# Optimization experiments

Hardware: AMD Instinct MI355X
Metric: run time of the kernel (lower is better)

The kernel has to match this reference:

```python
import jax, jax.numpy as jnp
import numpy as np

D_MODEL = 1024
D_STATE = 16
D_CONV = 4
EXPAND = 2
D_INNER = EXPAND * D_MODEL          # 2048
DT_RANK = D_MODEL // 16             # 64 (math.ceil(d_model/16))
BATCH, SEQLEN = 2, 1024


def setup_inputs() -> dict:
    key = jax.random.key(0)
    ks = jax.random.split(key, 9)
    f32 = jnp.float32
    hidden_states = jax.random.normal(ks[0], (BATCH, SEQLEN, D_MODEL), dtype=f32)
    in_proj_w = jax.random.normal(ks[1], (2 * D_INNER, D_MODEL), dtype=f32) * (D_MODEL ** -0.5)
    conv1d_w = jax.random.normal(ks[2], (D_INNER, D_CONV), dtype=f32) * (D_CONV ** -0.5)
    conv1d_b = jax.random.normal(ks[3], (D_INNER,), dtype=f32) * 0.1
    x_proj_w = jax.random.normal(ks[4], (DT_RANK + 2 * D_STATE, D_INNER), dtype=f32) * (D_INNER ** -0.5)
    dt_std = DT_RANK ** -0.5
    dt_proj_w = jax.random.uniform(ks[5], (D_INNER, DT_RANK), dtype=f32, minval=-dt_std, maxval=dt_std)
    dt_proj_b = jax.random.normal(ks[6], (D_INNER,), dtype=f32) * 0.1
    # A = repeat(arange(1, d_state+1), 'n -> d n'); A_log = log(A)
    A_log = jnp.log(jnp.tile(jnp.arange(1, D_STATE + 1, dtype=f32), (D_INNER, 1)))
    D_param = jnp.ones((D_INNER,), dtype=f32)
    out_proj_w = jax.random.normal(ks[7], (D_MODEL, D_INNER), dtype=f32) * (D_INNER ** -0.5)
    return dict(hidden_states=hidden_states, in_proj_w=in_proj_w, conv1d_w=conv1d_w,
                conv1d_b=conv1d_b, x_proj_w=x_proj_w, dt_proj_w=dt_proj_w,
                dt_proj_b=dt_proj_b, A_log=A_log, D_param=D_param, out_proj_w=out_proj_w)


def _mamba_fwd(hidden_states, in_proj_w, conv1d_w, conv1d_b, x_proj_w,
               dt_proj_w, dt_proj_b, A_log, D_param, out_proj_w):
    Bsz, L, _ = hidden_states.shape
    # in_proj: (B,L,d_model) -> (B,L,2*d_inner); split into x, z
    xz = jnp.einsum('bld,ed->ble', hidden_states, in_proj_w)
    x, z = jnp.split(xz, 2, axis=-1)                      # each (B,L,d_inner)
    # causal depthwise conv1d over L (left pad d_conv-1), then SiLU (fused in causal_conv1d_fwd)
    xc = jnp.transpose(x, (0, 2, 1))                      # (B,d_inner,L)
    kern = conv1d_w[:, None, :]                           # (d_inner,1,d_conv)
    conv = jax.lax.conv_general_dilated(
        xc, kern, window_strides=(1,), padding=[(D_CONV - 1, 0)],
        dimension_numbers=('NCH', 'OIH', 'NCH'), feature_group_count=D_INNER)
    u = jax.nn.silu(conv + conv1d_b[None, :, None])       # (B,d_inner,L)
    ut = jnp.transpose(u, (0, 2, 1))                      # (B,L,d_inner)
    # x_proj -> [dt | B | C]
    x_dbl = jnp.einsum('bld,rd->blr', ut, x_proj_w)       # (B,L,dt_rank+2*d_state)
    dt_low = x_dbl[..., :DT_RANK]
    B_var = x_dbl[..., DT_RANK:DT_RANK + D_STATE]         # (B,L,d_state)
    C_var = x_dbl[..., DT_RANK + D_STATE:]                # (B,L,d_state)
    # delta = softplus(dt_proj_w @ dt_low + dt_proj_b)  (delta_bias applied inside selective scan)
    delta = jax.nn.softplus(jnp.einsum('blr,dr->bld', dt_low, dt_proj_w) + dt_proj_b)  # (B,L,d_inner)
    A = -jnp.exp(A_log)                                   # (d_inner,d_state)
    # discretize: h_l = exp(delta*A) * h_{l-1} + (delta*B_l) * u_l
    dA = jnp.exp(delta[..., None] * A)                    # (B,L,d_inner,d_state)
    dBu = delta[..., None] * B_var[:, :, None, :] * ut[..., None]  # (B,L,d_inner,d_state)

    def step(h, inp):
        da, dbu, c = inp
        h = da * h + dbu                                  # (B,d_inner,d_state)
        y = jnp.einsum('bdn,bn->bd', h, c)
        return h, y

    h0 = jnp.zeros((Bsz, D_INNER, D_STATE), dtype=hidden_states.dtype)
    _, ys = jax.lax.scan(step, h0, (jnp.moveaxis(dA, 1, 0),
                                    jnp.moveaxis(dBu, 1, 0),
                                    jnp.moveaxis(C_var, 1, 0)))
    y = jnp.moveaxis(ys, 0, 1)                            # (B,L,d_inner)
    y = y + ut * D_param                                  # skip term D*u
    out_z = y * jax.nn.silu(z)                            # gated output
    return jnp.einsum('bld,ed->ble', out_z, out_proj_w)   # (B,L,d_model)


def reference(hidden_states, in_proj_w, conv1d_w, conv1d_b, x_proj_w,
              dt_proj_w, dt_proj_b, A_log, D_param, out_proj_w):
    return _mamba_fwd(hidden_states, in_proj_w, conv1d_w, conv1d_b, x_proj_w,
                      dt_proj_w, dt_proj_b, A_log, D_param, out_proj_w)
```

## Files before the change

### kernel.cpp

```cpp
#include <hip/hip_runtime.h>
#include <hip/hip_bf16.h>

#define BATCH 2
#define SEQLEN 1024
#define DMODEL 1024
#define DINNER 2048
#define DSTATE 16
#define DTRANK 64
#define ROWS (BATCH * SEQLEN)
#define LOG2E 1.44269504088896340736f

using bf16 = __hip_bfloat16;
typedef __bf16 bf16x8 __attribute__((ext_vector_type(8)));
typedef float f32x4 __attribute__((ext_vector_type(4)));
typedef unsigned short us8 __attribute__((ext_vector_type(8)));

__device__ __forceinline__ float to_f(float x) { return x; }
__device__ __forceinline__ float to_f(bf16 x) { return __bfloat162float(x); }

__device__ __forceinline__ float fexp2(float x) { return __builtin_amdgcn_exp2f(x); }

__device__ __forceinline__ float bfu(unsigned short u) {
    union { unsigned int i; float f; } v;
    v.i = ((unsigned int)u) << 16;
    return v.f;
}

__device__ __forceinline__ unsigned short bf_bits(float x) {
    bf16 h = __float2bfloat16(x);
    union { bf16 b; unsigned short u; } cv;
    cv.b = h;
    return cv.u;
}

__device__ __forceinline__ float softplus_f(float x) {
    return fmaxf(x, 0.f) + log1pf(expf(-fabsf(x)));
}
__device__ __forceinline__ float silu_f(float x) {
    return x * __builtin_amdgcn_rcpf(1.f + fexp2(-x * LOG2E));
}

__device__ __forceinline__ void gload16(const void* g, void* l) {
    __builtin_amdgcn_global_load_lds(
        (const __attribute__((address_space(1))) void*)g,
        (__attribute__((address_space(3))) void*)l, 16, 0, 0);
}

__global__ __launch_bounds__(256) void prep_kernel(const unsigned short* hs, int* flag,
                                                   float* zbuf, int nzero) {
    if (blockIdx.x == 0) {
        __shared__ int cnt[256];
        int c = 0;
        for (int i = threadIdx.x; i < 8192; i += 256) {
            int e = (hs[i] >> 7) & 0xFF;
            if (e == 0 || e == 0xFF || e < 96 || e > 159) c++;
        }
        cnt[threadIdx.x] = c;
        __syncthreads();
        for (int s = 128; s > 0; s >>= 1) {
            if (threadIdx.x < s) cnt[threadIdx.x] += cnt[threadIdx.x + s];
            __syncthreads();
        }
        if (threadIdx.x == 0) *flag = (cnt[0] < 512) ? 1 : 0;
    } else {
        int i = (blockIdx.x - 1) * 256 + threadIdx.x;
        if (i < nzero) zbuf[i] = 0.f;
    }
}

struct SrcPtrs { const void* p[10]; };

__device__ __constant__ const size_t SEG_OFF[11] = {
    0, 2097152, 6291456, 6299648, 6301696, 6498304,
    6629376, 6631424, 6664192, 6666240, 8763392
};

__global__ __launch_bounds__(256) void convert_all(SrcPtrs s, bf16* __restrict__ dst,
                                                   const int* __restrict__ flag) {
    size_t e = ((size_t)blockIdx.x * 256 + threadIdx.x) * 4;
    if (e >= SEG_OFF[10]) return;
    int seg = 0;
    #pragma unroll
    for (int i = 1; i < 10; ++i) if (e >= SEG_OFF[i]) seg = i;
    size_t loc = e - SEG_OFF[seg];
    if (*flag) {
        ushort4 v = ((const ushort4*)s.p[seg])[loc / 4];
        ((ushort4*)(dst + e))[0] = v;
    } else {
        float4 v = ((const float4*)s.p[seg])[loc / 4];
        ushort4 o;
        o.x = bf_bits(v.x); o.y = bf_bits(v.y);
        o.z = bf_bits(v.z); o.w = bf_bits(v.w);
        ((ushort4*)(dst + e))[0] = o;
    }
}

template <int OUTMODE>
__global__ __launch_bounds__(256) void gemm_mfma(
    const bf16* __restrict__ A, int lda,
    const bf16* __restrict__ Bm, int ldb,
    void* __restrict__ C, int ldc,
    int Kspl, size_t pstride,
    const bf16* __restrict__ bias)
{
    __shared__ __align__(16) __bf16 sA[128 * 32];
    __shared__ __align__(16) __bf16 sB[128 * 32];
    const int tid = threadIdx.x;
    const int m0 = blockIdx.y * 128;
    const int n0 = blockIdx.x * 128;
    const int wid = tid >> 6, ln = tid & 63;
    const int wy = (wid >> 1) * 64, wx = (wid & 1) * 64;
    const int q = ln >> 4, m16 = ln & 15;
    const int kbeg = blockIdx.z * Kspl;

    f32x4 acc[4][4] = {};

    for (int k0 = kbeg; k0 < kbeg + Kspl; k0 += 32) {
        #pragma unroll
        for (int i = 0; i < 2; ++i) {
            int idx = tid + i * 256;
            int r = idx >> 2, c = (idx & 3) * 8;
            gload16(&A[(size_t)(m0 + r) * lda + k0 + c], &sA[idx * 8]);
        }
        #pragma unroll
        for (int i = 0; i < 2; ++i) {
            int idx = tid + i * 256;
            int r = idx >> 2, c = (idx & 3) * 8;
            gload16(&Bm[(size_t)(n0 + r) * ldb + k0 + c], &sB[idx * 8]);
        }
        __syncthreads();
        bf16x8 a[4], b[4];
        #pragma unroll
        for (int i = 0; i < 4; ++i)
            a[i] = *(const bf16x8*)&sA[(wy + i * 16 + m16) * 32 + q * 8];
        #pragma unroll
        for (int j = 0; j < 4; ++j)
            b[j] = *(const bf16x8*)&sB[(wx + j * 16 + m16) * 32 + q * 8];
        #pragma unroll
        for (int i = 0; i < 4; ++i)
            #pragma unroll
            for (int j = 0; j < 4; ++j)
                acc[i][j] = __builtin_amdgcn_mfma_f32_16x16x32_bf16(a[i], b[j], acc[i][j], 0, 0, 0);
        __syncthreads();
    }

    #pragma unroll
    for (int i = 0; i < 4; ++i) {
        #pragma unroll
        for (int j = 0; j < 4; ++j) {
            #pragma unroll
            for (int r = 0; r < 4; ++r) {
                int row = m0 + wy + i * 16 + q * 4 + r;
                int col = n0 + wx + j * 16 + m16;
                size_t idx = (size_t)row * ldc + col;
                float v = acc[i][j][r];
                if constexpr (OUTMODE == 0) {
                    ((bf16*)C)[idx] = __float2bfloat16(v);
                } else if constexpr (OUTMODE == 2) {
                    ((float*)C + blockIdx.z * pstride)[idx] = v;
                } else if constexpr (OUTMODE == 3) {
                    if (col < 96) atomicAdd((float*)C + idx, v);
                } else if constexpr (OUTMODE == 4) {
                    ((float*)C)[idx] = softplus_f(v + to_f(bias[row]));
                }
            }
        }
    }
}

__global__ __launch_bounds__(256) void sum_store(
    const float* __restrict__ p0, const float* __restrict__ p1,
    void* __restrict__ out, const int* __restrict__ flag, int n4)
{
    int i = blockIdx.x * 256 + threadIdx.x;
    if (i >= n4) return;
    float4 a = ((const float4*)p0)[i];
    float4 b = ((const float4*)p1)[i];
    float4 sv; sv.x = a.x + b.x; sv.y = a.y + b.y; sv.z = a.z + b.z; sv.w = a.w + b.w;
    if (*flag) {
        ushort4 o;
        o.x = bf_bits(sv.x); o.y = bf_bits(sv.y);
        o.z = bf_bits(sv.z); o.w = bf_bits(sv.w);
        ((ushort4*)out)[i] = o;
    } else {
        ((float4*)out)[i] = sv;
    }
}

__global__ __launch_bounds__(256) void transpose_bf16(
    const ushort* __restrict__ src,
    ushort* __restrict__ dst)
{
    __shared__ ushort t[64][65];
    const int bx = blockIdx.x;
    const int by = blockIdx.y;
    const int tid = threadIdx.x;
    const int lr = tid & 63;
    const int ld = tid >> 6;
    #pragma unroll
    for (int i = 0; i < 16; ++i) {
        int d = ld + i * 4;
        t[d][lr] = src[(size_t)(by * 64 + d) * ROWS + bx * 64 + lr];
    }
    __syncthreads();
    #pragma unroll
    for (int i = 0; i < 16; ++i) {
        int r = ld + i * 4;
        dst[(size_t)(bx * 64 + r) * DINNER + by * 64 + lr] = t[lr][r];
    }
}

__global__ __launch_bounds__(256) void xd_post(
    const float* __restrict__ xd,
    float* __restrict__ xdT,
    bf16* __restrict__ xd_bf)
{
    __shared__ float t[96][65];
    const int row0 = blockIdx.x * 64;
    const int tid = threadIdx.x;
    for (int i = tid; i < 64 * 96; i += 256) {
        int row = i / 96, r = i - row * 96;
        float v = xd[(size_t)(row0 + row) * 96 + r];
        t[r][row] = v;
        xd_bf[(size_t)(row0 + row) * 96 + r] = __float2bfloat16(v);
    }
    __syncthreads();
    for (int i = tid; i < 96 * 64; i += 256) {
        int r = i >> 6, row = i & 63;
        xdT[(size_t)r * ROWS + row0 + row] = t[r][row];
    }
}

__global__ __launch_bounds__(256) void conv_silu_T8(
    const bf16* __restrict__ xzT,
    const bf16* __restrict__ w,
    const bf16* __restrict__ bias,
    bf16* __restrict__ utT)
{
    int t = blockIdx.x * 256 + threadIdx.x;
    int r0 = (t * 8) & (ROWS - 1);
    int d = t >> 8;

    const ushort* xp = (const ushort*)xzT + (size_t)d * ROWS + r0;
    float x[11];
    us8 cur = *(const us8*)xp;
    #pragma unroll
    for (int j = 0; j < 8; ++j) x[3 + j] = bfu(cur[j]);
    if ((r0 & (SEQLEN - 1)) != 0) {
        ushort4 pv = *(const ushort4*)(xp - 4);
        x[0] = bfu(pv.y); x[1] = bfu(pv.z); x[2] = bfu(pv.w);
    } else {
        x[0] = x[1] = x[2] = 0.f;
    }

    ushort4 wv = *(const ushort4*)((const ushort*)w + d * 4);
    float w0 = bfu(wv.x), w1 = bfu(wv.y), w2 = bfu(wv.z), w3 = bfu(wv.w);
    float bv = to_f(bias[d]);

    us8 o;
    #pragma unroll
    for (int j = 0; j < 8; ++j) {
        float acc = bv;
        acc = fmaf(x[j],     w0, acc);
        acc = fmaf(x[j + 1], w1, acc);
        acc = fmaf(x[j + 2], w2, acc);
        acc = fmaf(x[j + 3], w3, acc);
        o[j] = bf_bits(silu_f(acc));
    }
    *(us8*)((ushort*)utT + (size_t)d * ROWS + r0) = o;
}

#define SCHUNK 16
#define SSTEPS (SEQLEN / SCHUNK)
__global__ __launch_bounds__(1024) void scan_kernel8(
    const float* __restrict__ deltaT,
    const bf16*  __restrict__ utT,
    const float* __restrict__ xdT,
    const bf16*  __restrict__ xzT,
    const bf16*  __restrict__ A_log,
    const bf16*  __restrict__ Dp,
    bf16* __restrict__ outz)
{
    __shared__ float sH[SCHUNK][64], sP[SCHUNK][64];
    const int tid = threadIdx.x;
    const int c = tid >> 6;
    const int w = tid & 63;
    const int n = tid & 15;
    const int b = blockIdx.x >> 9;
    const int d = ((blockIdx.x & 511) << 2) + ((tid >> 4) & 3);
    const int row0 = b * SEQLEN + c * SSTEPS;

    const float Aa2 = -expf(to_f(A_log[d * DSTATE + n])) * LOG2E;
    const float Dv16 = to_f(Dp[d]) * (1.f / 16.f);

    const float*  dp = deltaT + (size_t)d * ROWS + row0;
    const ushort* up = (const ushort*)utT + (size_t)d * ROWS + row0;
    const ushort* zp = (const ushort*)xzT + (size_t)(DINNER + d) * ROWS + row0;
    const float*  Bp = xdT + (size_t)(64 + n) * ROWS + row0;
    const float*  Cp = xdT + (size_t)(80 + n) * ROWS + row0;

    float h = 0.f, sd = 0.f;
    {
        float4  dv4 = *(const float4*)(dp);
        ushort4 uv4 = *(const ushort4*)(up);
        float4  Bv4 = *(const float4*)(Bp);
        for (int i0 = 0; i0 < SSTEPS; i0 += 4) {
            float4 dvc = dv4; ushort4 uvc = uv4; float4 Bvc = Bv4;
            if (i0 + 4 < SSTEPS) {
                dv4 = *(const float4*)(dp + i0 + 4);
                uv4 = *(const ushort4*)(up + i0 + 4);
                Bv4 = *(const float4*)(Bp + i0 + 4);
            }
            float dv[4] = {dvc.x, dvc.y, dvc.z, dvc.w};
            float uv[4] = {bfu(uvc.x), bfu(uvc.y), bfu(uvc.z), bfu(uvc.w)};
            float Bv[4] = {Bvc.x, Bvc.y, Bvc.z, Bvc.w};
            #pragma unroll
            for (int j = 0; j < 4; ++j) {
                float a = fexp2(dv[j] * Aa2);
                h = fmaf(a, h, dv[j] * Bv[j] * uv[j]);
                sd += dv[j];
            }
        }
    }
    sH[c][w] = h;
    sP[c][w] = fexp2(sd * Aa2);
    __syncthreads();

    float hin = 0.f;
    for (int cc = 0; cc < c; ++cc)
        hin = fmaf(sP[cc][w], hin, sH[cc][w]);

    h = hin;
    {
        float4  dv4 = *(const float4*)(dp);
        ushort4 uv4 = *(const ushort4*)(up);
        float4  Bv4 = *(const float4*)(Bp);
        float4  Cv4 = *(const float4*)(Cp);
        ushort4 zv4 = *(const ushort4*)(zp);
        for (int i0 = 0; i0 < SSTEPS; i0 += 4) {
            float4 dvc = dv4; ushort4 uvc = uv4; float4 Bvc = Bv4;
            float4 Cvc = Cv4; ushort4 zvc = zv4;
            if (i0 + 4 < SSTEPS) {
                dv4 = *(const float4*)(dp + i0 + 4);
                uv4 = *(const ushort4*)(up + i0 + 4);
                Bv4 = *(const float4*)(Bp + i0 + 4);
                Cv4 = *(const float4*)(Cp + i0 + 4);
                zv4 = *(const ushort4*)(zp + i0 + 4);
            }
            float dv[4] = {dvc.x, dvc.y, dvc.z, dvc.w};
            float uv[4] = {bfu(uvc.x), bfu(uvc.y), bfu(uvc.z), bfu(uvc.w)};
            float Bv[4] = {Bvc.x, Bvc.y, Bvc.z, Bvc.w};
            float Cv[4] = {Cvc.x, Cvc.y, Cvc.z, Cvc.w};
            float zv[4] = {bfu(zvc.x), bfu(zvc.y), bfu(zvc.z), bfu(zvc.w)};
            float y[4];
            #pragma unroll
            for (int j = 0; j < 4; ++j) {
                float a = fexp2(dv[j] * Aa2);
                h = fmaf(a, h, dv[j] * Bv[j] * uv[j]);
                float p = fmaf(uv[j], Dv16, h * Cv[j]);
                p += __shfl_xor(p, 1, 16);
                p += __shfl_xor(p, 2, 16);
                p += __shfl_xor(p, 4, 16);
                p += __shfl_xor(p, 8, 16);
                y[j] = p;
            }
            float t0 = (n & 4) ? y[1] : y[0];
            float t1 = (n & 4) ? y[3] : y[2];
            float yv = (n & 8) ? t1 : t0;
            float z0 = (n & 4) ? zv[1] : zv[0];
            float z1 = (n & 4) ? zv[3] : zv[2];
            float zz = (n & 8) ? z1 : z0;
            if ((n & 3) == 0) {
                int q2 = n >> 2;
                outz[(size_t)(row0 + i0 + q2) * DINNER + d] =
                    __float2bfloat16(yv * silu_f(zz));
            }
        }
    }
}

extern "C" void kernel_launch(void* const* d_in, const int* in_sizes, int n_in,
                              void* d_out, int out_size, void* d_ws, size_t ws_size,
                              hipStream_t stream) {
    static const size_t SZ[10] = {
        (size_t)BATCH * SEQLEN * DMODEL,
        (size_t)2 * DINNER * DMODEL,
        (size_t)DINNER * 4,
        (size_t)DINNER,
        (size_t)(DTRANK + 2 * DSTATE) * DINNER,
        (size_t)DINNER * DTRANK,
        (size_t)DINNER,
        (size_t)DINNER * DSTATE,
        (size_t)DINNER,
        (size_t)DMODEL * DINNER
    };
    size_t tot_in = 0;
    for (int i = 0; i < 10; ++i) tot_in += SZ[i];

    char* p = (char*)d_ws;
    int* flag = (int*)p;                     p += 64;
    bf16* inb = (bf16*)p;                    p += tot_in * 2;
    bf16* xzT = (bf16*)p;                    p += (size_t)4096 * ROWS * 2;
    bf16* utT = (bf16*)p;                    p += (size_t)DINNER * ROWS * 2;
    bf16* ut  = (bf16*)p;                    p += (size_t)ROWS * DINNER * 2;
    float* xd = (float*)p;                   p += (size_t)ROWS * 96 * 4;
    bf16* xd_bf = (bf16*)p;                  p += (size_t)ROWS * 96 * 2;
    float* xdT = (float*)p;                  p += (size_t)96 * ROWS * 4;
    float* deltaT = (float*)p;               p += (size_t)DINNER * ROWS * 4;
    bf16* outz = (bf16*)p;                   p += (size_t)ROWS * DINNER * 2;
    float* part = (float*)p;                 p += (size_t)2 * ROWS * DMODEL * 4;
    size_t needed = (size_t)(p - (char*)d_ws);
    if (ws_size < needed) return;

    dim3 blk(256);

    prep_kernel<<<1 + (ROWS * 96 + 255) / 256, blk, 0, stream>>>(
        (const unsigned short*)d_in[0], flag, xd, ROWS * 96);

    bf16* inp[10];
    {
        size_t off = 0;
        for (int i = 0; i < 10; ++i) { inp[i] = inb + off; off += SZ[i]; }
    }
    SrcPtrs sp;
    for (int i = 0; i < 10; ++i) sp.p[i] = d_in[i];
    convert_all<<<(int)((tot_in / 4 + 255) / 256), blk, 0, stream>>>(sp, inb, flag);

    const bf16* hs        = inp[0];
    const bf16* in_proj_w = inp[1];
    const bf16* conv_w    = inp[2];
    const bf16* conv_b    = inp[3];
    const bf16* x_proj_w  = inp[4];
    const bf16* dt_proj_w = inp[5];
    const bf16* dt_proj_b = inp[6];
    const bf16* A_log     = inp[7];
    const bf16* Dp        = inp[8];
    const bf16* out_proj_w= inp[9];

    gemm_mfma<0><<<dim3(ROWS / 128, 4096 / 128, 1), blk, 0, stream>>>(
        in_proj_w, DMODEL, hs, DMODEL, xzT, ROWS, DMODEL, 0, nullptr);

    conv_silu_T8<<<(DINNER * ROWS / 8) / 256, blk, 0, stream>>>(xzT, conv_w, conv_b, utT);

    transpose_bf16<<<dim3(ROWS / 64, DINNER / 64), blk, 0, stream>>>(
        (const ushort*)utT, (ushort*)ut);

    gemm_mfma<3><<<dim3(1, ROWS / 128, 4), blk, 0, stream>>>(
        ut, DINNER, x_proj_w, DINNER, xd, 96, DINNER / 4, 0, nullptr);

    xd_post<<<ROWS / 64, blk, 0, stream>>>(xd, xdT, xd_bf);

    gemm_mfma<4><<<dim3(ROWS / 128, DINNER / 128, 1), blk, 0, stream>>>(
        dt_proj_w, DTRANK, xd_bf, 96, deltaT, ROWS, DTRANK, 0, dt_proj_b);

    scan_kernel8<<<BATCH * (DINNER / 4), dim3(1024), 0, stream>>>(
        deltaT, utT, xdT, xzT, A_log, Dp, outz);

    gemm_mfma<2><<<dim3(DMODEL / 128, ROWS / 128, 2), blk, 0, stream>>>(
        outz, DINNER, out_proj_w, DINNER, part, DMODEL, DINNER / 2, (size_t)ROWS * DMODEL, nullptr);

    sum_store<<<(ROWS * DMODEL / 4 + 255) / 256, blk, 0, stream>>>(
        part, part + (size_t)ROWS * DMODEL, d_out, flag, ROWS * DMODEL / 4);
}
```

Baseline: 349.4 us.

## Skip bf16 copies of large inputs, deepen scan prefetch, raise scan occupancy hint

When the inputs are already bf16, the convert kernel no longer copies the hidden states, in_proj and out_proj weights. The GEMMs read those inputs directly through alternate pointers chosen by a device flag. The scan kernel now prefetches two 4-step groups ahead instead of one and adds a minimum-blocks hint to launch bounds. The aim is to cut copy traffic and hide load latency in the scan, at the cost of extra registers and a flag read in every GEMM block.

```diff
diff --git a/kernel.cpp b/kernel.cpp
--- a/kernel.cpp
+++ b/kernel.cpp
@@ -82,8 +82,10 @@
     int seg = 0;
     #pragma unroll
     for (int i = 1; i < 10; ++i) if (e >= SEG_OFF[i]) seg = i;
+    int isbf = *flag;
+    if (isbf && (seg == 0 || seg == 1 || seg == 9)) return;
     size_t loc = e - SEG_OFF[seg];
-    if (*flag) {
+    if (isbf) {
         ushort4 v = ((const ushort4*)s.p[seg])[loc / 4];
         ((ushort4*)(dst + e))[0] = v;
     } else {
@@ -101,8 +103,15 @@
     const bf16* __restrict__ Bm, int ldb,
     void* __restrict__ C, int ldc,
     int Kspl, size_t pstride,
-    const bf16* __restrict__ bias)
-{
+    const bf16* __restrict__ bias,
+    const bf16* __restrict__ Aalt,
+    const bf16* __restrict__ Balt,
+    const int* __restrict__ flag)
+{
+    if (flag && *flag) {
+        if (Aalt) A = Aalt;
+        if (Balt) Bm = Balt;
+    }
     __shared__ __align__(16) __bf16 sA[128 * 32];
     __shared__ __align__(16) __bf16 sB[128 * 32];
     const int tid = threadIdx.x;
@@ -272,7 +281,7 @@
 
 #define SCHUNK 16
 #define SSTEPS (SEQLEN / SCHUNK)
-__global__ __launch_bounds__(1024) void scan_kernel8(
+__global__ __launch_bounds__(1024, 8) void scan_kernel9(
     const float* __restrict__ deltaT,
     const bf16*  __restrict__ utT,
     const float* __restrict__ xdT,
@@ -301,15 +310,19 @@
 
     float h = 0.f, sd = 0.f;
     {
-        float4  dv4 = *(const float4*)(dp);
-        ushort4 uv4 = *(const ushort4*)(up);
-        float4  Bv4 = *(const float4*)(Bp);
+        float4  d0 = *(const float4*)(dp);
+        ushort4 u0 = *(const ushort4*)(up);
+        float4  B0 = *(const float4*)(Bp);
+        float4  d1 = *(const float4*)(dp + 4);
+        ushort4 u1 = *(const ushort4*)(up + 4);
+        float4  B1 = *(const float4*)(Bp + 4);
         for (int i0 = 0; i0 < SSTEPS; i0 += 4) {
-            float4 dvc = dv4; ushort4 uvc = uv4; float4 Bvc = Bv4;
-            if (i0 + 4 < SSTEPS) {
-                dv4 = *(const float4*)(dp + i0 + 4);
-                uv4 = *(const ushort4*)(up + i0 + 4);
-                Bv4 = *(const float4*)(Bp + i0 + 4);
+            float4 dvc = d0; ushort4 uvc = u0; float4 Bvc = B0;
+            d0 = d1; u0 = u1; B0 = B1;
+            if (i0 + 8 < SSTEPS) {
+                d1 = *(const float4*)(dp + i0 + 8);
+                u1 = *(const ushort4*)(up + i0 + 8);
+                B1 = *(const float4*)(Bp + i0 + 8);
             }
             float dv[4] = {dvc.x, dvc.y, dvc.z, dvc.w};
             float uv[4] = {bfu(uvc.x), bfu(uvc.y), bfu(uvc.z), bfu(uvc.w)};
@@ -332,20 +345,26 @@
 
     h = hin;
     {
-        float4  dv4 = *(const float4*)(dp);
-        ushort4 uv4 = *(const ushort4*)(up);
-        float4  Bv4 = *(const float4*)(Bp);
-        float4  Cv4 = *(const float4*)(Cp);
-        ushort4 zv4 = *(const ushort4*)(zp);
+        float4  d0 = *(const float4*)(dp);
+        ushort4 u0 = *(const ushort4*)(up);
+        float4  B0 = *(const float4*)(Bp);
+        float4  C0 = *(const float4*)(Cp);
+        ushort4 z0 = *(const ushort4*)(zp);
+        float4  d1 = *(const float4*)(dp + 4);
+        ushort4 u1 = *(const ushort4*)(up + 4);
+        float4  B1 = *(const float4*)(Bp + 4);
+        float4  C1 = *(const float4*)(Cp + 4);
+        ushort4 z1 = *(const ushort4*)(zp + 4);
         for (int i0 = 0; i0 < SSTEPS; i0 += 4) {
-            float4 dvc = dv4; ushort4 uvc = uv4; float4 Bvc = Bv4;
-            float4 Cvc = Cv4; ushort4 zvc = zv4;
-            if (i0 + 4 < SSTEPS) {
-                dv4 = *(const float4*)(dp + i0 + 4);
-                uv4 = *(const ushort4*)(up + i0 + 4);
-                Bv4 = *(const float4*)(Bp + i0 + 4);
-                Cv4 = *(const float4*)(Cp + i0 + 4);
-                zv4 = *(const ushort4*)(zp + i0 + 4);
+            float4 dvc = d0; ushort4 uvc = u0; float4 Bvc = B0;
+            float4 Cvc = C0; ushort4 zvc = z0;
+            d0 = d1; u0 = u1; B0 = B1; C0 = C1; z0 = z1;
+            if (i0 + 8 < SSTEPS) {
+                d1 = *(const float4*)(dp + i0 + 8);
+                u1 = *(const ushort4*)(up + i0 + 8);
+                B1 = *(const float4*)(Bp + i0 + 8);
+                C1 = *(const float4*)(Cp + i0 + 8);
+                z1 = *(const ushort4*)(zp + i0 + 8);
             }
             float dv[4] = {dvc.x, dvc.y, dvc.z, dvc.w};
             float uv[4] = {bfu(uvc.x), bfu(uvc.y), bfu(uvc.z), bfu(uvc.w)};
@@ -367,9 +386,9 @@
             float t0 = (n & 4) ? y[1] : y[0];
             float t1 = (n & 4) ? y[3] : y[2];
             float yv = (n & 8) ? t1 : t0;
-            float z0 = (n & 4) ? zv[1] : zv[0];
-            float z1 = (n & 4) ? zv[3] : zv[2];
-            float zz = (n & 8) ? z1 : z0;
+            float za = (n & 4) ? zv[1] : zv[0];
+            float zb = (n & 4) ? zv[3] : zv[2];
+            float zz = (n & 8) ? zb : za;
             if ((n & 3) == 0) {
                 int q2 = n >> 2;
                 outz[(size_t)(row0 + i0 + q2) * DINNER + d] =
@@ -438,7 +457,8 @@
     const bf16* out_proj_w= inp[9];
 
     gemm_mfma<0><<<dim3(ROWS / 128, 4096 / 128, 1), blk, 0, stream>>>(
-        in_proj_w, DMODEL, hs, DMODEL, xzT, ROWS, DMODEL, 0, nullptr);
+        in_proj_w, DMODEL, hs, DMODEL, xzT, ROWS, DMODEL, 0, nullptr,
+        (const bf16*)d_in[1], (const bf16*)d_in[0], flag);
 
     conv_silu_T8<<<(DINNER * ROWS / 8) / 256, blk, 0, stream>>>(xzT, conv_w, conv_b, utT);
 
@@ -446,18 +466,21 @@
         (const ushort*)utT, (ushort*)ut);
 
     gemm_mfma<3><<<dim3(1, ROWS / 128, 4), blk, 0, stream>>>(
-        ut, DINNER, x_proj_w, DINNER, xd, 96, DINNER / 4, 0, nullptr);
+        ut, DINNER, x_proj_w, DINNER, xd, 96, DINNER / 4, 0, nullptr,
+        nullptr, nullptr, nullptr);
 
     xd_post<<<ROWS / 64, blk, 0, stream>>>(xd, xdT, xd_bf);
 
     gemm_mfma<4><<<dim3(ROWS / 128, DINNER / 128, 1), blk, 0, stream>>>(
-        dt_proj_w, DTRANK, xd_bf, 96, deltaT, ROWS, DTRANK, 0, dt_proj_b);
-
-    scan_kernel8<<<BATCH * (DINNER / 4), dim3(1024), 0, stream>>>(
+        dt_proj_w, DTRANK, xd_bf, 96, deltaT, ROWS, DTRANK, 0, dt_proj_b,
+        nullptr, nullptr, nullptr);
+
+    scan_kernel9<<<BATCH * (DINNER / 4), dim3(1024), 0, stream>>>(
         deltaT, utT, xdT, xzT, A_log, Dp, outz);
 
     gemm_mfma<2><<<dim3(DMODEL / 128, ROWS / 128, 2), blk, 0, stream>>>(
-        outz, DINNER, out_proj_w, DINNER, part, DMODEL, DINNER / 2, (size_t)ROWS * DMODEL, nullptr);
+        outz, DINNER, out_proj_w, DINNER, part, DMODEL, DINNER / 2, (size_t)ROWS * DMODEL,
+        nullptr, nullptr, (const bf16*)d_in[9], flag);
 
     sum_store<<<(ROWS * DMODEL / 4 + 255) / 256, blk, 0, stream>>>(
         part, part + (size_t)ROWS * DMODEL, d_out, flag, ROWS * DMODEL / 4);
```

New measurement: 398.6 us. 14.1% more time.
